# Optimization experiments

Measured on AMD Instinct MI355X. Metric: run time of the kernel, lower is better.

Reference implementation:

```python
import jax, jax.numpy as jnp
import numpy as np
from jax import lax

DN = ('NCDHW', 'OIDHW', 'NCDHW')
BN_EPS = 1e-5  # eval-mode BatchNorm3d with running_mean=0, running_var=1


def conv3d(x, w, b):
    y = lax.conv_general_dilated(x, w, window_strides=(1, 1, 1),
                                 padding=[(1, 1)] * 3, dimension_numbers=DN)
    return y + b[None, :, None, None, None]


def maxpool2(x):
    return lax.reduce_window(x, -jnp.inf, lax.max,
                             (1, 1, 2, 2, 2), (1, 1, 2, 2, 2), 'VALID')


def spline_block(x, cw, cb, knots, sw, w1, w2, g, beta):
    # SplineConv3d: conv -> (BSpline3D blend with SiLU) -> BN(eval) -> maxpool
    y = conv3d(x, cw, cb)                                   # [b,c,d,h,w]
    basis = jnp.maximum(y[..., None] - knots, 0.0) ** 3     # [b,c,d,h,w,k]
    sp = jnp.einsum('bcdhwk,ck->bcdhw', basis, sw)
    out = (w1[None, :, None, None, None] * sp
           + w2[None, :, None, None, None] * (y * jax.nn.sigmoid(y)))
    scale = (g / jnp.sqrt(1.0 + BN_EPS))[None, :, None, None, None]
    return maxpool2(out * scale + beta[None, :, None, None, None])


def setup_inputs() -> dict:
    key = jax.random.key(0)
    ks = iter(jax.random.split(key, 40))
    def nrm(shape, s=1.0):
        return jax.random.normal(next(ks), shape, dtype=jnp.float32) * s
    d = {}
    d['x'] = nrm((2, 1, 64, 64, 64))
    for cin, cout, t in [(1, 32, '1'), (32, 64, '2'), (64, 128, '3')]:
        d[f'c{t}_w'] = nrm((cout, cin, 3, 3, 3), 0.1)
        d[f'c{t}_b'] = nrm((cout,), 0.01)
        d[f'c{t}_knots'] = jnp.linspace(-1.0, 1.0, 10).astype(jnp.float32)
        d[f'c{t}_sw'] = nrm((cout, 10), 0.2)
        d[f'c{t}_w1'] = nrm((cout,), 0.2)
        d[f'c{t}_w2'] = nrm((cout,), 0.2)
        d[f'bn{t}_g'] = 1.0 + nrm((cout,), 0.1)
        d[f'bn{t}_b'] = nrm((cout,), 0.1)
    d['fc1_w'] = nrm((256, 128), 0.05)
    d['fc1_b'] = nrm((256,), 0.01)
    d['fc2_w'] = nrm((2, 256), 0.05)
    d['fc2_b'] = nrm((2,), 0.01)
    return d


def reference(x,
              c1_w, c1_b, c1_knots, c1_sw, c1_w1, c1_w2, bn1_g, bn1_b,
              c2_w, c2_b, c2_knots, c2_sw, c2_w1, c2_w2, bn2_g, bn2_b,
              c3_w, c3_b, c3_knots, c3_sw, c3_w1, c3_w2, bn3_g, bn3_b,
              fc1_w, fc1_b, fc2_w, fc2_b):
    h = spline_block(x, c1_w, c1_b, c1_knots, c1_sw, c1_w1, c1_w2, bn1_g, bn1_b)
    h = spline_block(h, c2_w, c2_b, c2_knots, c2_sw, c2_w1, c2_w2, bn2_g, bn2_b)
    h = spline_block(h, c3_w, c3_b, c3_knots, c3_sw, c3_w1, c3_w2, bn3_g, bn3_b)
    h = h.mean(axis=(2, 3, 4))          # AdaptiveAvgPool3d((1,1,1)) + flatten
    h = jax.nn.relu(h @ fc1_w.T + fc1_b)  # dropout is identity in eval mode
    return h @ fc2_w.T + fc2_b
```

## Files before the change

kernel.cpp:

```cpp
#include <hip/hip_runtime.h>
#include <math.h>


#define GLOBAL_AS __attribute__((address_space(1)))
#define LDS_AS    __attribute__((address_space(3)))

static __device__ __forceinline__ void async_ld16(const float* g, float* l) {
    __builtin_amdgcn_global_load_lds((const GLOBAL_AS void*)g, (LDS_AS void*)l,
                                     16, 0, 0);
}

__global__ __launch_bounds__(256) void repack_kernel(
    const float* __restrict__ w1, const float* __restrict__ w2,
    const float* __restrict__ w3,
    float* __restrict__ o1, float* __restrict__ o2, float* __restrict__ o3,
    float* __restrict__ zbuf, float* __restrict__ pooled,
    float* __restrict__ cntf)
{
    const int i = blockIdx.x * 256 + threadIdx.x;
    const float* src;
    float* dst;
    if (i < 32)            { src = w1 + i * 27;           dst = o1 + i * 28; }
    else if (i < 2080)     { const int j = i - 32;   src = w2 + j * 27; dst = o2 + j * 28; }
    else if (i < 10272)    { const int j = i - 2080; src = w3 + j * 27; dst = o3 + j * 28; }
    else {
        if (i < 10288) zbuf[i - 10272] = 0.0f;
        else if (i < 10544) pooled[i - 10288] = 0.0f;
        else if (i < 10560) cntf[i - 10544] = 0.0f;
        return;
    }
#pragma unroll
    for (int t = 0; t < 27; t++) dst[t] = src[t];
    dst[27] = 0.0f;
}

template <int TPB_, int CIN, int CSPLIT, int G,
          int WDT, int WHT, int WWT, int BD, int BH, int BW, bool FMEAN>
__global__ __launch_bounds__(TPB_, 2) void spline_block_kernel(
    const float* __restrict__ x,
    const float4* __restrict__ wpk,
    const float* __restrict__ cb,
    const float* __restrict__ knots,
    const float* __restrict__ sw,
    const float* __restrict__ w1,
    const float* __restrict__ w2,
    const float* __restrict__ g,
    const float* __restrict__ beta,
    const float* __restrict__ zbuf,
    float* __restrict__ out,
    const float* __restrict__ fw1, const float* __restrict__ fb1,
    const float* __restrict__ fw2, const float* __restrict__ fb2,
    float* __restrict__ dout, int* __restrict__ cnt,
    int N, int Cout, int D, int H, int W,
    int ntiles, int nthw, int ntw)
{
    constexpr int NSW    = BD * BH * BW;
    constexpr int NW     = TPB_ / 64;
    constexpr int CPG    = CIN / CSPLIT;
    constexpr int ID     = 2 * WDT + 2;
    constexpr int IH     = 2 * WHT + 2;
    constexpr int CHK    = (WWT + 4) / 2;
    constexpr int PITCH  = CHK * 4;
    constexpr int ROWS   = ID * IH;
    constexpr int CHUNKS = ROWS * CHK;
    constexpr int PHYS   = CHUNKS * 4;
    constexpr int NCH    = (CHUNKS + 63) / 64;
    constexpr int BUFS   = (CPG > 1) ? 2 : 1;
    static_assert(NW == NSW * CSPLIT, "waves = spatial-tiles x cin-split");
    static_assert(WDT * WHT * WWT == 64, "one wave per spatial tile");
    static_assert(CIN % CSPLIT == 0, "cin divisible");
    static_assert(G == 4 || G == 8, "acc layout assumes G in {4,8}");
    static_assert(NCH <= 32, "mask fits u32");
    static_assert(NCH == 6, "s_waitcnt vmcnt(6) literal assumes 6 issues/cin");
    static_assert(CSPLIT == 1 ||
                  (CSPLIT - 1) * NSW * 64 * G * 8 <= NW * BUFS * PHYS,
                  "reduction scratch fits in tile");
    static_assert(!FMEAN || TPB_ == 256, "fused fc assumes 256 threads");

    __shared__ __align__(16) float tile[NW][BUFS][PHYS];
    __shared__ float4 stbl[G * 11];
    __shared__ int lastblk;

    const int PD = D >> 1, PH = H >> 1, PW = W >> 1;
    const int groups = Cout / G;
    const int tid  = threadIdx.x;
    const int wv   = tid >> 6;
    const int lane = tid & 63;
    const int sw_  = wv % NSW;
    const int cg   = wv / NSW;

    const int bx      = blockIdx.x;
    const int tile_id = bx % ntiles;
    const int t1      = bx / ntiles;
    const int grp     = t1 % groups;
    const int n       = t1 / groups;
    const int c0      = grp * G;
    const int cinbase = cg * CPG;
    const int cinbase_u = __builtin_amdgcn_readfirstlane(cinbase);

    const int td  = tile_id / nthw;
    const int rem = tile_id % nthw;
    const int th_ = rem / ntw;
    const int tw_ = rem % ntw;

    for (int i = tid; i < G * 11; i += TPB_) {
        const int gg  = i / 11;
        const int cnt2 = i % 11;
        const int c   = c0 + gg;
        float A = 0.f, B3 = 0.f, C3 = 0.f, Dd = 0.f;
        for (int j = 0; j < cnt2; j++) {
            const float s = sw[c * 10 + j];
            const float k = knots[j];
            A  += s;
            B3 += 3.0f * s * k;
            C3 += 3.0f * s * k * k;
            Dd += s * k * k * k;
        }
        stbl[i] = make_float4(A, B3, C3, Dd);
    }

    const int swd = sw_ / (BH * BW);
    const int r2  = sw_ % (BH * BW);
    const int swh = r2 / BW;
    const int sww = r2 % BW;
    const int pd0 = td  * (BD * WDT) + swd * WDT;
    const int ph0 = th_ * (BH * WHT) + swh * WHT;
    const int pw0 = tw_ * (BW * WWT) + sww * WWT;

    const int pwl = lane % WWT;
    const int phl = (lane / WWT) % WHT;
    const int pdl = lane / (WWT * WHT);

    const int d0 = 2 * pd0 - 1, h0 = 2 * ph0 - 1;
    const int w0 = 2 * pw0 - 1;
    const int wb = w0 & ~3;
    const int woff = w0 - wb;

    int off[NCH];
    unsigned vm = 0;
#pragma unroll
    for (int k = 0; k < NCH; k++) {
        const int chunk = lane + 64 * k;
        const int row = chunk / CHK, cs = chunk - row * CHK;
        const int dz = row / IH, hy = row - dz * IH;
        const int dd = d0 + dz, hh = h0 + hy;
        const int wsd = wb + cs * 4;
        const bool ok = (chunk < CHUNKS) &
                        ((unsigned)dd < (unsigned)D) &
                        ((unsigned)hh < (unsigned)H) &
                        ((unsigned)wsd < (unsigned)W);
        off[k] = ok ? (dd * H + hh) * W + wsd : 0;
        vm |= (unsigned)ok << k;
    }

    const size_t chstride = (size_t)D * H * W;
    const float* xn = x + (size_t)n * CIN * chstride;

    float acc[G][8];
#pragma unroll
    for (int gg = 0; gg < G; gg++)
#pragma unroll
        for (int i = 0; i < 8; i++) acc[gg][i] = 0.0f;

    __syncthreads();

    auto stage = [&](int ci, int buf) {
        const float* xc = xn + (size_t)ci * chstride;
        float* dst = &tile[wv][buf][0];
#pragma unroll
        for (int k = 0; k < NCH; k++) {
            const int chunk = lane + 64 * k;
            if ((k + 1) * 64 <= CHUNKS || chunk < CHUNKS) {
                const float* src = ((vm >> k) & 1) ? (xc + off[k]) : zbuf;
                async_ld16(src, dst + chunk * 4);
            }
        }
    };

    stage(cinbase, 0);

#pragma unroll 1
    for (int s = 0; s < CPG; s++) {
        const int cur = s & (BUFS - 1);
        if (s + 1 < CPG) {
            stage(cinbase + s + 1, cur ^ 1);
            asm volatile("s_waitcnt vmcnt(6)" ::: "memory");
        } else {
            asm volatile("s_waitcnt vmcnt(0)" ::: "memory");
        }

        const int ci_u = cinbase_u + s;
        const float* tb = &tile[wv][cur][0];
        float r[64];
#pragma unroll
        for (int dz = 0; dz < 4; dz++)
#pragma unroll
        for (int dy = 0; dy < 4; dy++) {
            const int rb = ((2 * pdl + dz) * IH + (2 * phl + dy)) * PITCH +
                           woff + 2 * pwl;
            r[(dz * 4 + dy) * 4 + 0] = tb[rb + 0];
            r[(dz * 4 + dy) * 4 + 1] = tb[rb + 1];
            r[(dz * 4 + dy) * 4 + 2] = tb[rb + 2];
            r[(dz * 4 + dy) * 4 + 3] = tb[rb + 3];
        }

#pragma unroll
        for (int gg = 0; gg < G; gg++) {
            const float4* wq = wpk + ((size_t)(c0 + gg) * CIN + ci_u) * 7;
            float4 q[7];
#pragma unroll
            for (int ch = 0; ch < 7; ch++) q[ch] = wq[ch];
#pragma unroll
            for (int ch = 0; ch < 7; ch++) {
#pragma unroll
                for (int j = 0; j < 4; j++) {
                    const int tap = ch * 4 + j;
                    if (tap < 27) {
                        const float wvj = (j == 0) ? q[ch].x : (j == 1) ? q[ch].y
                                        : (j == 2) ? q[ch].z : q[ch].w;
                        const int kd = tap / 9, kh = (tap % 9) / 3, kw = tap % 3;
#pragma unroll
                        for (int od = 0; od < 2; od++)
#pragma unroll
                        for (int oh = 0; oh < 2; oh++)
#pragma unroll
                        for (int ow = 0; ow < 2; ow++)
                            acc[gg][(od * 2 + oh) * 2 + ow] =
                                fmaf(wvj,
                                     r[((od + kd) * 4 + (oh + kh)) * 4 + (ow + kw)],
                                     acc[gg][(od * 2 + oh) * 2 + ow]);
                    }
                }
            }
        }
    }

    float* af = &acc[0][0];
    if (CSPLIT > 1) {
        __syncthreads();
        float* scratch = &tile[0][0][0];
        if (cg > 0) {
#pragma unroll
            for (int idx = 0; idx < G * 8; idx++)
                scratch[((idx * (CSPLIT - 1) + (cg - 1)) * NSW + sw_) * 64 + lane]
                    = af[idx];
        }
        __syncthreads();
        if (cg == 0) {
#pragma unroll
            for (int idx = 0; idx < G * 8; idx++) {
                float s2 = af[idx];
                for (int j = 0; j < CSPLIT - 1; j++)
                    s2 += scratch[((idx * (CSPLIT - 1) + j) * NSW + sw_) * 64 + lane];
                af[idx] = s2;
            }
        }
    }

    if (cg == 0) {
        const int pdg = pd0 + pdl, phg = ph0 + phl, pwg = pw0 + pwl;
        const float inv_vol = 1.0f / (float)(PD * PH * PW);
#pragma unroll
        for (int gg = 0; gg < G; gg++) {
            const int c = c0 + gg;
            const float bias = cb[c];
            const float W1 = w1[c], W2 = w2[c];
            const float scale = g[c] * rsqrtf(1.0f + 1e-5f);
            const float bb = beta[c];
            float m = -INFINITY;
#pragma unroll
            for (int i = 0; i < 8; i++) {
                const float y = acc[gg][i] + bias;
                int idx = (int)floorf((y + 1.0f) * 4.5f) + 1;
                idx = min(max(idx, 0), 10);
                const float4 cf = stbl[gg * 11 + idx];
                const float sp = ((cf.x * y - cf.y) * y + cf.z) * y - cf.w;
                const float silu = y / (1.0f + __expf(-y));
                const float o = fmaf(W1 * sp + W2 * silu, scale, bb);
                m = fmaxf(m, o);
            }
            if constexpr (FMEAN) {
                float ssum = m;
#pragma unroll
                for (int o2 = 32; o2 > 0; o2 >>= 1)
                    ssum += __shfl_down(ssum, o2, 64);
                if (lane == 0)
                    atomicAdd(&out[(size_t)n * Cout + c], ssum * inv_vol);
            } else {
                out[((size_t)(n * Cout + c) * PD + pdg) * PH * PW +
                    phg * PW + pwg] = m;
            }
        }
    }

    if constexpr (FMEAN) {
        __syncthreads();
        if (tid == 0) {
            __threadfence();
            lastblk = (atomicAdd(cnt, 1) == (int)gridDim.x - 1);
        }
        __syncthreads();
        if (lastblk) {
            __threadfence();
            float* fl = &tile[0][0][0];
            fl[tid] = atomicAdd(&out[tid], 0.0f);
            __syncthreads();
#pragma unroll
            for (int nn = 0; nn < 2; nn++) {
                float s = fb1[tid];
                for (int k = 0; k < 128; k++)
                    s = fmaf(fl[nn * 128 + k], fw1[tid * 128 + k], s);
                fl[256 + nn * 256 + tid] = fmaxf(s, 0.0f);
            }
            __syncthreads();
            const int wid = tid >> 6, l2 = tid & 63;
            const int nn = wid >> 1, oo = wid & 1;
            float s = 0.0f;
            for (int k = l2; k < 256; k += 64)
                s += fl[256 + nn * 256 + k] * fw2[oo * 256 + k];
#pragma unroll
            for (int o2 = 32; o2 > 0; o2 >>= 1) s += __shfl_down(s, o2, 64);
            if (l2 == 0) dout[nn * 2 + oo] = s + fb2[oo];
        }
    }
}

extern "C" void kernel_launch(void* const* d_in, const int* in_sizes, int n_in,
                              void* d_out, int out_size, void* d_ws, size_t ws_size,
                              hipStream_t stream) {
    const float* x      = (const float*)d_in[0];
    const float* c1_w   = (const float*)d_in[1];
    const float* c1_b   = (const float*)d_in[2];
    const float* c1_kn  = (const float*)d_in[3];
    const float* c1_sw  = (const float*)d_in[4];
    const float* c1_w1  = (const float*)d_in[5];
    const float* c1_w2  = (const float*)d_in[6];
    const float* bn1_g  = (const float*)d_in[7];
    const float* bn1_b  = (const float*)d_in[8];
    const float* c2_w   = (const float*)d_in[9];
    const float* c2_b   = (const float*)d_in[10];
    const float* c2_kn  = (const float*)d_in[11];
    const float* c2_sw  = (const float*)d_in[12];
    const float* c2_w1  = (const float*)d_in[13];
    const float* c2_w2  = (const float*)d_in[14];
    const float* bn2_g  = (const float*)d_in[15];
    const float* bn2_b  = (const float*)d_in[16];
    const float* c3_w   = (const float*)d_in[17];
    const float* c3_b   = (const float*)d_in[18];
    const float* c3_kn  = (const float*)d_in[19];
    const float* c3_sw  = (const float*)d_in[20];
    const float* c3_w1  = (const float*)d_in[21];
    const float* c3_w2  = (const float*)d_in[22];
    const float* bn3_g  = (const float*)d_in[23];
    const float* bn3_b  = (const float*)d_in[24];
    const float* fc1_w  = (const float*)d_in[25];
    const float* fc1_b  = (const float*)d_in[26];
    const float* fc2_w  = (const float*)d_in[27];
    const float* fc2_b  = (const float*)d_in[28];

    float* ws = (float*)d_ws;
    float* h1     = ws;
    float* h2     = h1 + 2097152;
    float* pooled = h2 + 524288;
    float* zbuf   = pooled + 256;
    float* cntf   = zbuf + 16;
    float* wp1    = cntf + 16;
    float* wp2    = wp1 + 896;
    float* wp3    = wp2 + 57344;

    repack_kernel<<<dim3(42), dim3(256), 0, stream>>>(
        c1_w, c2_w, c3_w, wp1, wp2, wp3, zbuf, pooled, cntf);

    spline_block_kernel<256, 1, 1, 4, 2, 4, 8, 2, 2, 1, false>
        <<<dim3(2048), dim3(256), 0, stream>>>(
        x, (const float4*)wp1, c1_b, c1_kn, c1_sw, c1_w1, c1_w2, bn1_g, bn1_b,
        zbuf, h1, nullptr, nullptr, nullptr, nullptr, nullptr, nullptr,
        2, 32, 64, 64, 64, 128, 16, 4);
    spline_block_kernel<256, 32, 2, 8, 2, 4, 8, 1, 1, 2, false>
        <<<dim3(512), dim3(256), 0, stream>>>(
        h1, (const float4*)wp2, c2_b, c2_kn, c2_sw, c2_w1, c2_w2, bn2_g, bn2_b,
        zbuf, h2, nullptr, nullptr, nullptr, nullptr, nullptr, nullptr,
        2, 64, 32, 32, 32, 32, 4, 1);
    spline_block_kernel<256, 64, 4, 4, 2, 4, 8, 1, 1, 1, true>
        <<<dim3(512), dim3(256), 0, stream>>>(
        h2, (const float4*)wp3, c3_b, c3_kn, c3_sw, c3_w1, c3_w2, bn3_g, bn3_b,
        zbuf, pooled, fc1_w, fc1_b, fc2_w, fc2_b, (float*)d_out, (int*)cntf,
        2, 128, 16, 16, 16, 8, 2, 1);
}
```

Before: 318.5 us.

## Add direct-global-load spline kernel without LDS staging for first two layers

Adds a new spline conv kernel that loads each thread's 4x4x4 input patch straight from global memory into registers. It skips the LDS tile staging and the cin-split reduction. Layers 1 and 2 now use it, with layer 2 also changing from G=8 with a channel split to G=4 with a 2x2 spatial arrangement. The goal is to remove LDS traffic and barriers, at the cost of redundant global and cache reads between neighbouring threads and fewer waves per output for layer 2.

```diff
diff --git a/kernel.cpp b/kernel.cpp
--- a/kernel.cpp
+++ b/kernel.cpp
@@ -32,6 +32,185 @@
 #pragma unroll
     for (int t = 0; t < 27; t++) dst[t] = src[t];
     dst[27] = 0.0f;
+}
+
+template <int TPB_, int CIN, int G, int WDT, int WHT, int WWT,
+          int BD, int BH, int BW>
+__global__ __launch_bounds__(TPB_, 2) void spline_direct_kernel(
+    const float* __restrict__ x,
+    const float4* __restrict__ wpk,
+    const float* __restrict__ cb,
+    const float* __restrict__ knots,
+    const float* __restrict__ sw,
+    const float* __restrict__ w1,
+    const float* __restrict__ w2,
+    const float* __restrict__ g,
+    const float* __restrict__ beta,
+    const float* __restrict__ zbuf,
+    float* __restrict__ out,
+    int N, int Cout, int D, int H, int W,
+    int ntiles, int nthw, int ntw)
+{
+    constexpr int NSW = BD * BH * BW;
+    constexpr int NW  = TPB_ / 64;
+    static_assert(NW == NSW, "one wave per spatial tile, no cin-split");
+    static_assert(WDT * WHT * WWT == 64, "wave tile = 64 outputs");
+    static_assert(G == 4, "acc layout assumes G==4");
+
+    __shared__ float4 stbl[G * 11];
+
+    const int PD = D >> 1, PH = H >> 1, PW = W >> 1;
+    const int groups = Cout / G;
+    const int tid  = threadIdx.x;
+    const int wv   = tid >> 6;
+    const int lane = tid & 63;
+
+    const int bx      = blockIdx.x;
+    const int tile_id = bx % ntiles;
+    const int t1      = bx / ntiles;
+    const int grp     = t1 % groups;
+    const int n       = t1 / groups;
+    const int c0      = grp * G;
+
+    const int td  = tile_id / nthw;
+    const int rem = tile_id % nthw;
+    const int th_ = rem / ntw;
+    const int tw_ = rem % ntw;
+
+    for (int i = tid; i < G * 11; i += TPB_) {
+        const int gg  = i / 11;
+        const int cnt = i % 11;
+        const int c   = c0 + gg;
+        float A = 0.f, B3 = 0.f, C3 = 0.f, Dd = 0.f;
+        for (int j = 0; j < cnt; j++) {
+            const float s = sw[c * 10 + j];
+            const float k = knots[j];
+            A  += s;
+            B3 += 3.0f * s * k;
+            C3 += 3.0f * s * k * k;
+            Dd += s * k * k * k;
+        }
+        stbl[i] = make_float4(A, B3, C3, Dd);
+    }
+
+    const int swd = wv / (BH * BW);
+    const int r2  = wv % (BH * BW);
+    const int swh = r2 / BW;
+    const int sww = r2 % BW;
+    const int pd0 = td  * (BD * WDT) + swd * WDT;
+    const int ph0 = th_ * (BH * WHT) + swh * WHT;
+    const int pw0 = tw_ * (BW * WWT) + sww * WWT;
+
+    const int pwl = lane % WWT;
+    const int phl = (lane / WWT) % WHT;
+    const int pdl = lane / (WWT * WHT);
+
+    const int ddb = 2 * (pd0 + pdl) - 1;
+    const int hhb = 2 * (ph0 + phl) - 1;
+    const int wwb = 2 * (pw0 + pwl) - 1;
+
+    int dzo[4], dyo[4];
+    unsigned okd = 0, okh = 0, okw = 0;
+#pragma unroll
+    for (int dz = 0; dz < 4; dz++) {
+        const int dd = ddb + dz;
+        okd |= (unsigned)((unsigned)dd < (unsigned)D) << dz;
+        dzo[dz] = dd * H * W;
+    }
+#pragma unroll
+    for (int dy = 0; dy < 4; dy++) {
+        const int hh = hhb + dy;
+        okh |= (unsigned)((unsigned)hh < (unsigned)H) << dy;
+        dyo[dy] = hh * W;
+    }
+#pragma unroll
+    for (int j = 0; j < 4; j++)
+        okw |= (unsigned)((unsigned)(wwb + j) < (unsigned)W) << j;
+
+    const size_t chstride = (size_t)D * H * W;
+
+    float acc[G][8];
+#pragma unroll
+    for (int gg = 0; gg < G; gg++)
+#pragma unroll
+        for (int i = 0; i < 8; i++) acc[gg][i] = 0.0f;
+
+    __syncthreads();
+
+#pragma unroll 1
+    for (int s = 0; s < CIN; s++) {
+        const float* xc = x + ((size_t)n * CIN + s) * chstride;
+
+        float r[64];
+#pragma unroll
+        for (int dz = 0; dz < 4; dz++)
+#pragma unroll
+        for (int dy = 0; dy < 4; dy++) {
+            const bool rok = ((okd >> dz) & 1) & ((okh >> dy) & 1);
+            const int rb = dzo[dz] + dyo[dy] + wwb;
+#pragma unroll
+            for (int j = 0; j < 4; j++) {
+                const bool ok = rok & (bool)((okw >> j) & 1);
+                const float* p = ok ? (xc + rb + j) : zbuf;
+                r[(dz * 4 + dy) * 4 + j] = *p;
+            }
+        }
+
+#pragma unroll
+        for (int gg = 0; gg < G; gg++) {
+            const float4* wq = wpk + ((size_t)(c0 + gg) * CIN + s) * 7;
+            float4 q[7];
+#pragma unroll
+            for (int ch = 0; ch < 7; ch++) q[ch] = wq[ch];
+#pragma unroll
+            for (int ch = 0; ch < 7; ch++) {
+#pragma unroll
+                for (int j = 0; j < 4; j++) {
+                    const int tap = ch * 4 + j;
+                    if (tap < 27) {
+                        const float wvj = (j == 0) ? q[ch].x : (j == 1) ? q[ch].y
+                                        : (j == 2) ? q[ch].z : q[ch].w;
+                        const int kd = tap / 9, kh = (tap % 9) / 3, kw = tap % 3;
+#pragma unroll
+                        for (int od = 0; od < 2; od++)
+#pragma unroll
+                        for (int oh = 0; oh < 2; oh++)
+#pragma unroll
+                        for (int ow = 0; ow < 2; ow++)
+                            acc[gg][(od * 2 + oh) * 2 + ow] =
+                                fmaf(wvj,
+                                     r[((od + kd) * 4 + (oh + kh)) * 4 + (ow + kw)],
+                                     acc[gg][(od * 2 + oh) * 2 + ow]);
+                    }
+                }
+            }
+        }
+    }
+
+    {
+        const int pdg = pd0 + pdl, phg = ph0 + phl, pwg = pw0 + pwl;
+#pragma unroll
+        for (int gg = 0; gg < G; gg++) {
+            const int c = c0 + gg;
+            const float bias = cb[c];
+            const float W1 = w1[c], W2 = w2[c];
+            const float scale = g[c] * rsqrtf(1.0f + 1e-5f);
+            const float bb = beta[c];
+            float m = -INFINITY;
+#pragma unroll
+            for (int i = 0; i < 8; i++) {
+                const float y = acc[gg][i] + bias;
+                int idx = (int)floorf((y + 1.0f) * 4.5f) + 1;
+                idx = min(max(idx, 0), 10);
+                const float4 cf = stbl[gg * 11 + idx];
+                const float sp = ((cf.x * y - cf.y) * y + cf.z) * y - cf.w;
+                const float silu = y / (1.0f + __expf(-y));
+                const float o = fmaf(W1 * sp + W2 * silu, scale, bb);
+                m = fmaxf(m, o);
+            }
+            out[((size_t)(n * Cout + c) * PD + pdg) * PH * PW + phg * PW + pwg] = m;
+        }
+    }
 }
 
 template <int TPB_, int CIN, int CSPLIT, int G,
@@ -69,8 +248,7 @@
     static_assert(NW == NSW * CSPLIT, "waves = spatial-tiles x cin-split");
     static_assert(WDT * WHT * WWT == 64, "one wave per spatial tile");
     static_assert(CIN % CSPLIT == 0, "cin divisible");
-    static_assert(G == 4 || G == 8, "acc layout assumes G in {4,8}");
-    static_assert(NCH <= 32, "mask fits u32");
+    static_assert(G == 4, "acc layout assumes G==4");
     static_assert(NCH == 6, "s_waitcnt vmcnt(6) literal assumes 6 issues/cin");
     static_assert(CSPLIT == 1 ||
                   (CSPLIT - 1) * NSW * 64 * G * 8 <= NW * BUFS * PHYS,
@@ -371,16 +549,14 @@
     repack_kernel<<<dim3(42), dim3(256), 0, stream>>>(
         c1_w, c2_w, c3_w, wp1, wp2, wp3, zbuf, pooled, cntf);
 
-    spline_block_kernel<256, 1, 1, 4, 2, 4, 8, 2, 2, 1, false>
+    spline_direct_kernel<256, 1, 4, 2, 4, 8, 2, 2, 1>
         <<<dim3(2048), dim3(256), 0, stream>>>(
         x, (const float4*)wp1, c1_b, c1_kn, c1_sw, c1_w1, c1_w2, bn1_g, bn1_b,
-        zbuf, h1, nullptr, nullptr, nullptr, nullptr, nullptr, nullptr,
-        2, 32, 64, 64, 64, 128, 16, 4);
-    spline_block_kernel<256, 32, 2, 8, 2, 4, 8, 1, 1, 2, false>
+        zbuf, h1, 2, 32, 64, 64, 64, 128, 16, 4);
+    spline_direct_kernel<256, 32, 4, 2, 4, 8, 2, 2, 1>
         <<<dim3(512), dim3(256), 0, stream>>>(
         h1, (const float4*)wp2, c2_b, c2_kn, c2_sw, c2_w1, c2_w2, bn2_g, bn2_b,
-        zbuf, h2, nullptr, nullptr, nullptr, nullptr, nullptr, nullptr,
-        2, 64, 32, 32, 32, 32, 4, 1);
+        zbuf, h2, 2, 64, 32, 32, 32, 16, 4, 2);
     spline_block_kernel<256, 64, 4, 4, 2, 4, 8, 1, 1, 1, true>
         <<<dim3(512), dim3(256), 0, stream>>>(
         h2, (const float4*)wp3, c3_b, c3_kn, c3_sw, c3_w1, c3_w2, bn3_g, bn3_b,
```

Result: slower. 478.9 us (+50.4%).
